# Optimization experiments

Hardware: AMD Instinct MI355X
Metric: run time of the kernel (lower is better)

The kernel has to match this reference:

```python
import jax, jax.numpy as jnp
import numpy as np

# Standard SMPL kinematic tree parents (kintree_table)
PARENTS = np.array([-1, 0, 0, 0, 1, 2, 3, 4, 5, 6, 7, 8, 9, 9, 9,
                    12, 13, 14, 16, 17, 18, 19, 20, 21])
NV, NJ, NB, NP = 6890, 24, 10, 207


def rodrigues(r):
    """Axis-angle [N,3] -> rotation matrices [N,3,3] (Rodrigues formula)."""
    theta = jnp.linalg.norm(r, axis=1, keepdims=True) + 1e-8  # [N,1]
    rh = r / theta                                            # [N,3]
    cos = jnp.cos(theta)[..., None]                           # [N,1,1]
    sin = jnp.sin(theta)[..., None]
    z = jnp.zeros_like(rh[:, 0])
    m = jnp.stack([z, -rh[:, 2], rh[:, 1],
                   rh[:, 2], z, -rh[:, 0],
                   -rh[:, 1], rh[:, 0], z], axis=1).reshape(-1, 3, 3)
    dot = rh[:, :, None] * rh[:, None, :]                     # outer product
    eye = jnp.eye(3, dtype=r.dtype)
    return cos * eye + (1.0 - cos) * dot + sin * m


def setup_inputs() -> dict:
    key = jax.random.key(0)
    ks = jax.random.split(key, 9)
    B = 512
    betas = jax.random.normal(ks[0], (B, NB), dtype=jnp.float32)
    thetas = jax.random.normal(ks[1], (B, NJ * 3), dtype=jnp.float32) * 0.3
    trans = jax.random.normal(ks[2], (B, 3), dtype=jnp.float32)
    scale = jnp.ones((1,), dtype=jnp.float32)
    v_template = jax.random.normal(ks[3], (NV, 3), dtype=jnp.float32)
    shapedirs = jax.random.normal(ks[4], (NV, 3, NB), dtype=jnp.float32) * 0.01
    posedirs = jax.random.normal(ks[5], (NV, 3, NP), dtype=jnp.float32) * 0.01
    Jr = jax.random.uniform(ks[6], (NJ, NV), dtype=jnp.float32)
    J_regressor = Jr / jnp.sum(Jr, axis=1, keepdims=True)
    w = jax.random.uniform(ks[7], (NV, NJ), dtype=jnp.float32)
    weights = w / jnp.sum(w, axis=1, keepdims=True)
    return {"betas": betas, "thetas": thetas, "trans": trans, "scale": scale,
            "v_template": v_template, "shapedirs": shapedirs,
            "posedirs": posedirs, "J_regressor": J_regressor,
            "weights": weights}


def reference(betas, thetas, trans, scale, v_template, shapedirs, posedirs,
              J_regressor, weights):
    B = betas.shape[0]
    dt = betas.dtype
    # Shape blend shapes: v_shaped [B, 6890, 3]
    v_shaped = jnp.einsum('bs,vcs->bvc', betas, shapedirs) + v_template
    # Rest-pose joints J(beta): [B, 24, 3]
    J = jnp.einsum('jv,bvc->bjc', J_regressor, v_shaped)
    # Local rotations from axis-angle, root scaled by `scale`
    lRs = rodrigues(thetas.reshape(-1, 3)).reshape(B, NJ, 3, 3)
    lRs = lRs.at[:, 0].multiply(scale[0])
    # Local joint offsets: root keeps J[:,0], children use J[i] - J[parent[i]]
    parents = jnp.asarray(PARENTS)
    t = J - J[:, jnp.clip(parents, 0)]
    t = t.at[:, 0].set(J[:, 0])
    # Local 4x4 transforms [B, 24, 4, 4]
    top = jnp.concatenate([lRs, t[..., None]], axis=3)          # [B,24,3,4]
    bottom = jnp.broadcast_to(jnp.array([0., 0., 0., 1.], dtype=dt),
                              (B, NJ, 1, 4))
    A = jnp.concatenate([top, bottom], axis=2)
    # Kinematic chain accumulation (fixed 24-joint tree)
    results = [A[:, 0]]
    for i in range(1, NJ):
        results.append(results[PARENTS[i]] @ A[:, i])
    stacked = jnp.stack(results, axis=1)                         # [B,24,4,4]
    # Remove rest-pose joint locations from translation column
    Jh = jnp.concatenate([J, jnp.zeros((B, NJ, 1), dtype=dt)], axis=2)
    deformed = jnp.einsum('bjxy,bjy->bjx', stacked, Jh)          # [B,24,4]
    G = stacked.at[..., 3].add(-deformed)
    # Pose blend shapes from non-root rotations
    lrotmin = (lRs[:, 1:] - jnp.eye(3, dtype=dt)).reshape(B, -1)  # [B,207]
    v_posed = v_shaped + jnp.einsum('bp,vcp->bvc', lrotmin, posedirs)
    # Linear blend skinning
    T = jnp.einsum('bjxy,vj->bvxy', G, weights)                  # [B,6890,4,4]
    vh = jnp.concatenate([v_posed, jnp.ones((B, NV, 1), dtype=dt)], axis=2)
    v = jnp.einsum('bvxy,bvy->bvx', T, vh)[:, :, :3]
    result = v + trans[:, None, :]
    joints = jnp.einsum('jv,bvc->bjc', J_regressor, result)
    return result, joints
```

## Files before the change

### kernel.cpp

```cpp
#include <hip/hip_runtime.h>

#define NVERT 6890
#define NJNT  24
#define NBETA 10
#define NPOSE 207
#define NBATCH 512
#define KPAD 224
#define MROWS 20736
#define NVC (NVERT * 3)

typedef __attribute__((ext_vector_type(8))) short short8;
typedef __attribute__((ext_vector_type(4))) float floatx4;

__constant__ int c_par[NJNT]   = {-1,0,0,0,1,2,3,4,5,6,7,8,9,9,9,12,13,14,16,17,18,19,20,21};
__constant__ int c_depth[NJNT] = { 0,1,1,1,2,2,2,3,3,3,4,4,4,4,4,5,5,5,6,6,7,7,8,8};

static __device__ __forceinline__ unsigned short f2bf(float x) {
  union { float f; unsigned u; } v; v.f = x;
  unsigned r = (v.u + 0x7FFFu + ((v.u >> 16) & 1u)) >> 16;
  return (unsigned short)r;
}
static __device__ __forceinline__ float bf2f(unsigned short h) {
  union { unsigned u; float f; } v; v.u = (unsigned)h << 16;
  return v.f;
}

__global__ __launch_bounds__(256) void k_buildA(
    const float* __restrict__ pdir, const float* __restrict__ sd,
    const float* __restrict__ vt, unsigned short* __restrict__ AT) {
  const int idx = blockIdx.x * 256 + threadIdx.x;
  const int row = idx / KPAD, k = idx - row * KPAD;
  float val = 0.f;
  if (row < NVC) {
    if (k < NPOSE)            val = pdir[(size_t)row * NPOSE + k];
    else if (k < NPOSE + 10)  val = sd[(size_t)row * 10 + (k - NPOSE)];
    else if (k == NPOSE + 10) val = vt[row];
  }
  AT[idx] = f2bf(val);
}

__global__ __launch_bounds__(256) void k_buildW(
    const float* __restrict__ wgt, unsigned short* __restrict__ W16) {
  const int idx = blockIdx.x * 256 + threadIdx.x;
  const int v = idx >> 6, c = idx & 63, j = c & 31, h = c >> 5;
  const float w = (v < NVERT && j < 24) ? wgt[(size_t)v * 24 + j] : 0.f;
  const unsigned short hi = f2bf(w);
  W16[idx] = h ? f2bf(w - bf2f(hi)) : hi;
}

__global__ __launch_bounds__(256) void k_jreg1(
    const float* __restrict__ Jr, const float* __restrict__ vt,
    const float* __restrict__ sd, float* __restrict__ wsJP) {
  const int jc = blockIdx.x, j = jc / 3, c = jc % 3;
  const int v0 = blockIdx.y * 864;
  const int vend = min(NVERT, v0 + 864);
  const int tid = threadIdx.x;
  float acc[11];
  #pragma unroll
  for (int k = 0; k < 11; ++k) acc[k] = 0.f;
  for (int v = v0 + tid; v < vend; v += 256) {
    const float w = Jr[j * NVERT + v];
    acc[0] += w * vt[v * 3 + c];
    const float* s = sd + (size_t)v * 30 + c * 10;
    #pragma unroll
    for (int k = 0; k < 10; ++k) acc[1 + k] += w * s[k];
  }
  #pragma unroll
  for (int off = 32; off > 0; off >>= 1) {
    #pragma unroll
    for (int k = 0; k < 11; ++k) acc[k] += __shfl_down(acc[k], off, 64);
  }
  __shared__ float red[4][11];
  const int lane = tid & 63, wv = tid >> 6;
  if (lane == 0) {
    #pragma unroll
    for (int k = 0; k < 11; ++k) red[wv][k] = acc[k];
  }
  __syncthreads();
  if (tid == 0) {
    #pragma unroll
    for (int k = 0; k < 11; ++k)
      wsJP[(size_t)(blockIdx.y * 72 + jc) * 11 + k] =
          red[0][k] + red[1][k] + red[2][k] + red[3][k];
  }
}

__global__ __launch_bounds__(256, 2) void k_chain3(
    const float* __restrict__ betas, const float* __restrict__ thetas,
    const float* __restrict__ scale, const float* __restrict__ trans,
    const float* __restrict__ wsJP,
    unsigned short* __restrict__ BT, unsigned short* __restrict__ G16) {
  __shared__ __align__(16) float sJ[792];
  __shared__ __align__(16) float sJJ[4][72];
  __shared__ __align__(16) float sM[4][288];
  __shared__ __align__(16) unsigned short sG[4][1024];
  __shared__ __align__(16) unsigned short sB[4][KPAD];

  const int tid = threadIdx.x;
  const int wv = tid >> 6, lane = tid & 63;
  const int b = blockIdx.x * 4 + wv;

  if (tid < 72) {
    #pragma unroll
    for (int k = 0; k < 11; ++k) {
      float s = 0.f;
      #pragma unroll
      for (int c8 = 0; c8 < 8; ++c8) s += wsJP[(size_t)(c8 * 72 + tid) * 11 + k];
      if (k == 0) sJ[tid] = s;
      else        sJ[72 + tid * 10 + (k - 1)] = s;
    }
  }
  #pragma unroll
  for (int r = 0; r < 4; ++r) {
    sG[wv][lane * 16 + r * 4 + 0] = 0; sG[wv][lane * 16 + r * 4 + 1] = 0;
    sG[wv][lane * 16 + r * 4 + 2] = 0; sG[wv][lane * 16 + r * 4 + 3] = 0;
  }
  __syncthreads();

  float R[9], t[3], M[12], Jx = 0.f, Jy = 0.f, Jz = 0.f;
  const int i = lane;
  if (i < NJNT) {
    #pragma unroll
    for (int c = 0; c < 3; ++c) {
      float a = sJ[i * 3 + c];
      const float* d = sJ + 72 + (i * 3 + c) * 10;
      #pragma unroll
      for (int s = 0; s < NBETA; ++s) a += d[s] * betas[b * NBETA + s];
      if (c == 0) Jx = a; else if (c == 1) Jy = a; else Jz = a;
    }
    sJJ[wv][i * 3 + 0] = Jx; sJJ[wv][i * 3 + 1] = Jy; sJJ[wv][i * 3 + 2] = Jz;
    const float rx = thetas[b * 72 + i * 3 + 0];
    const float ry = thetas[b * 72 + i * 3 + 1];
    const float rz = thetas[b * 72 + i * 3 + 2];
    const float th = sqrtf(rx * rx + ry * ry + rz * rz) + 1e-8f;
    const float inv = 1.f / th;
    const float x = rx * inv, y = ry * inv, z = rz * inv;
    const float cs = cosf(th), sn = sinf(th), omc = 1.f - cs;
    R[0] = cs + omc * x * x;     R[1] = omc * x * y - sn * z; R[2] = omc * x * z + sn * y;
    R[3] = omc * x * y + sn * z; R[4] = cs + omc * y * y;     R[5] = omc * y * z - sn * x;
    R[6] = omc * x * z - sn * y; R[7] = omc * y * z + sn * x; R[8] = cs + omc * z * z;
    if (i == 0) {
      const float sc = scale[0];
      #pragma unroll
      for (int k = 0; k < 9; ++k) R[k] *= sc;
    } else {
      #pragma unroll
      for (int k = 0; k < 9; ++k)
        sB[wv][(i - 1) * 9 + k] = f2bf(R[k] - ((k == 0 || k == 4 || k == 8) ? 1.f : 0.f));
    }
  }
  if (i == 0) {
    #pragma unroll
    for (int s = 0; s < NBETA; ++s) sB[wv][NPOSE + s] = f2bf(betas[b * NBETA + s]);
    sB[wv][NPOSE + 10] = 0x3F80;
    #pragma unroll
    for (int k = NPOSE + 11; k < KPAD; ++k) sB[wv][k] = 0;
  }
  __syncthreads();

  if (i < NJNT) {
    if (i == 0) { t[0] = Jx; t[1] = Jy; t[2] = Jz; }
    else {
      const int p = c_par[i];
      t[0] = Jx - sJJ[wv][p * 3 + 0];
      t[1] = Jy - sJJ[wv][p * 3 + 1];
      t[2] = Jz - sJJ[wv][p * 3 + 2];
    }
    if (i == 0) {
      #pragma unroll
      for (int r = 0; r < 3; ++r) {
        M[r*4+0] = R[r*3+0]; M[r*4+1] = R[r*3+1]; M[r*4+2] = R[r*3+2]; M[r*4+3] = t[r];
      }
      #pragma unroll
      for (int k = 0; k < 12; ++k) sM[wv][k] = M[k];
    }
  }
  __syncthreads();

  for (int lvl = 1; lvl <= 8; ++lvl) {
    if (i < NJNT && c_depth[i] == lvl) {
      const float* Mp = sM[wv] + c_par[i] * 12;
      #pragma unroll
      for (int r = 0; r < 3; ++r) {
        const float p0 = Mp[r*4+0], p1 = Mp[r*4+1], p2 = Mp[r*4+2], p3 = Mp[r*4+3];
        M[r*4+0] = p0*R[0] + p1*R[3] + p2*R[6];
        M[r*4+1] = p0*R[1] + p1*R[4] + p2*R[7];
        M[r*4+2] = p0*R[2] + p1*R[5] + p2*R[8];
        M[r*4+3] = p0*t[0] + p1*t[1] + p2*t[2] + p3;
      }
      #pragma unroll
      for (int k = 0; k < 12; ++k) sM[wv][i * 12 + k] = M[k];
    }
    __syncthreads();
  }

  if (i < NJNT) {
    #pragma unroll
    for (int r = 0; r < 3; ++r) {
      M[r*4+3] = M[r*4+3] - (M[r*4+0]*Jx + M[r*4+1]*Jy + M[r*4+2]*Jz)
               + trans[b * 3 + r];
    }
    #pragma unroll
    for (int e = 0; e < 12; ++e) {
      const float g = M[e];
      const unsigned short hi = f2bf(g);
      sG[wv][e * 32 + i]       = hi;
      sG[wv][512 + e * 32 + i] = f2bf(g - bf2f(hi));
    }
  }
  __syncthreads();

  *(uint4*)(G16 + (size_t)b * 1024 + lane * 16)     = *(uint4*)&sG[wv][lane * 16];
  *(uint4*)(G16 + (size_t)b * 1024 + lane * 16 + 8) = *(uint4*)&sG[wv][lane * 16 + 8];
  if (lane < 28)
    *(uint4*)(BT + (size_t)b * KPAD + lane * 8) = *(uint4*)&sB[wv][lane * 8];
}

__global__ __launch_bounds__(256, 3) void k_skin4(
    const unsigned short* __restrict__ AT, const unsigned short* __restrict__ BT,
    const unsigned short* __restrict__ W16, const unsigned short* __restrict__ G16,
    float* __restrict__ out) {
  __shared__ __align__(16) char smem[43776];
  unsigned short* sAs = (unsigned short*)smem;
  unsigned short* sBs = (unsigned short*)(smem + 15360);
  float* sV           = (float*)smem;
  unsigned short* sG2 = (unsigned short*)(smem + 13056);
  unsigned short* sWh = (unsigned short*)(smem + 33536);
  unsigned short* sWl = (unsigned short*)(smem + 38656);

  const int tid = threadIdx.x;
  const int wv = tid >> 6, lane = tid & 63;
  const int q = lane >> 4, n = lane & 15;
  const int b0 = blockIdx.x * 64;
  const int vc0 = blockIdx.y * 192;

  for (int i = tid; i < 512; i += 256) {
    const int row = i >> 3, c8 = i & 7;
    const uint4 w = *(const uint4*)(W16 + (size_t)(blockIdx.y * 64 + row) * 64 + c8 * 8);
    if (c8 < 4) *(uint4*)(sWh + row * 40 + c8 * 8) = w;
    else        *(uint4*)(sWl + row * 40 + (c8 - 4) * 8) = w;
  }

  floatx4 acc[3][4];
  #pragma unroll
  for (int mt = 0; mt < 3; ++mt)
    #pragma unroll
    for (int nt = 0; nt < 4; ++nt) acc[mt][nt] = (floatx4)(0.f);

  const int srow = tid >> 2, sj = tid & 3;
  for (int kt = 0; kt < 7; ++kt) {
    if (kt) __syncthreads();
    #pragma unroll
    for (int it = 0; it < 3; ++it) {
      const int row = it * 64 + srow;
      *(uint4*)(sAs + row * 40 + sj * 8) =
          *(const uint4*)(AT + (size_t)(vc0 + row) * KPAD + kt * 32 + sj * 8);
    }
    *(uint4*)(sBs + srow * 40 + sj * 8) =
        *(const uint4*)(BT + (size_t)(b0 + srow) * KPAD + kt * 32 + sj * 8);
    __syncthreads();
    short8 af[3], bfr[4];
    #pragma unroll
    for (int mt = 0; mt < 3; ++mt)
      af[mt] = *(const short8*)(sAs + (48 * wv + 16 * mt + n) * 40 + q * 8);
    #pragma unroll
    for (int nt = 0; nt < 4; ++nt)
      bfr[nt] = *(const short8*)(sBs + (16 * nt + n) * 40 + q * 8);
    #pragma unroll
    for (int mt = 0; mt < 3; ++mt)
      #pragma unroll
      for (int nt = 0; nt < 4; ++nt)
        acc[mt][nt] = __builtin_amdgcn_mfma_f32_16x16x32_bf16(
            af[mt], bfr[nt], acc[mt][nt], 0, 0, 0);
  }

  short8 wh[4], wl[4];
  #pragma unroll
  for (int vt = 0; vt < 4; ++vt) {
    wh[vt] = *(const short8*)(sWh + (vt * 16 + n) * 40 + q * 8);
    wl[vt] = *(const short8*)(sWl + (vt * 16 + n) * 40 + q * 8);
  }

  for (int nt = 0; nt < 4; ++nt) {
    for (int s = 0; s < 2; ++s) {
      __syncthreads();
      if (s == 0) {
        #pragma unroll
        for (int mt = 0; mt < 3; ++mt)
          #pragma unroll
          for (int r = 0; r < 4; ++r)
            sV[(48 * wv + 16 * mt + 4 * q + r) * 17 + n] = acc[mt][nt][r];
      }
      const int bg0 = b0 + nt * 16 + s * 8;
      for (int i = tid; i < 1024; i += 256) {
        const int row = i >> 2, c4 = i & 3;
        const int t = row >> 5, rem = row & 31;
        *(uint4*)(sG2 + row * 40 + c4 * 8) =
            *(const uint4*)(G16 + (size_t)(bg0 + t) * 1024 + rem * 32 + c4 * 8);
      }
      __syncthreads();
      #pragma unroll
      for (int bb = 0; bb < 2; ++bb) {
        const int t = wv * 2 + bb;
        const int col = s * 8 + t;
        const int bg = b0 + nt * 16 + col;
        const short8 gh = *(const short8*)(sG2 + (t * 32 + n) * 40 + q * 8);
        const short8 gl = *(const short8*)(sG2 + (t * 32 + 16 + n) * 40 + q * 8);
        #pragma unroll
        for (int vt = 0; vt < 4; ++vt) {
          floatx4 a2 = (floatx4)(0.f);
          a2 = __builtin_amdgcn_mfma_f32_16x16x32_bf16(gh, wl[vt], a2, 0, 0, 0);
          a2 = __builtin_amdgcn_mfma_f32_16x16x32_bf16(gl, wh[vt], a2, 0, 0, 0);
          a2 = __builtin_amdgcn_mfma_f32_16x16x32_bf16(gh, wh[vt], a2, 0, 0, 0);
          const float X = sV[(48 * vt + 3 * n + 0) * 17 + col];
          const float Y = sV[(48 * vt + 3 * n + 1) * 17 + col];
          const float Z = sV[(48 * vt + 3 * n + 2) * 17 + col];
          const float o = a2[0] * X + a2[1] * Y + a2[2] * Z + a2[3];
          const int vc = vc0 + 48 * vt + 3 * n + q;
          if (q < 3 && vc < NVC)
            out[(size_t)bg * NVC + vc] = o;
        }
      }
    }
  }
}

__global__ __launch_bounds__(256) void k_joints(
    const float* __restrict__ Jr, const float* __restrict__ res,
    float* __restrict__ joints) {
  const int b = blockIdx.x;
  const int lane = threadIdx.x & 63, wv = threadIdx.x >> 6;
  float acc[18];
  #pragma unroll
  for (int k = 0; k < 18; ++k) acc[k] = 0.f;
  const float* rb = res + (size_t)b * NVC;
  for (int v = lane; v < NVERT; v += 64) {
    const float r0 = rb[v*3+0], r1 = rb[v*3+1], r2 = rb[v*3+2];
    #pragma unroll
    for (int k = 0; k < 6; ++k) {
      const int j = wv + 4 * k;
      const float w = Jr[j * NVERT + v];
      acc[k*3+0] += w * r0; acc[k*3+1] += w * r1; acc[k*3+2] += w * r2;
    }
  }
  #pragma unroll
  for (int off = 32; off > 0; off >>= 1) {
    #pragma unroll
    for (int k = 0; k < 18; ++k) acc[k] += __shfl_down(acc[k], off, 64);
  }
  if (lane == 0) {
    #pragma unroll
    for (int k = 0; k < 6; ++k) {
      const int j = wv + 4 * k;
      joints[(size_t)b * 72 + j * 3 + 0] = acc[k*3+0];
      joints[(size_t)b * 72 + j * 3 + 1] = acc[k*3+1];
      joints[(size_t)b * 72 + j * 3 + 2] = acc[k*3+2];
    }
  }
}

extern "C" void kernel_launch(void* const* d_in, const int* in_sizes, int n_in,
                              void* d_out, int out_size, void* d_ws, size_t ws_size,
                              hipStream_t stream) {
  const float* betas  = (const float*)d_in[0];
  const float* thetas = (const float*)d_in[1];
  const float* trans  = (const float*)d_in[2];
  const float* scale  = (const float*)d_in[3];
  const float* vtpl   = (const float*)d_in[4];
  const float* sd     = (const float*)d_in[5];
  const float* pdir   = (const float*)d_in[6];
  const float* Jr     = (const float*)d_in[7];
  const float* wgt    = (const float*)d_in[8];
  float* out = (float*)d_out;

  float* ws   = (float*)d_ws;
  float* wsJP = ws;
  unsigned short* AT  = (unsigned short*)(ws + 6336);
  unsigned short* BT  = AT + (size_t)MROWS * KPAD;
  unsigned short* W16 = BT + (size_t)NBATCH * KPAD;
  unsigned short* G16 = W16 + (size_t)6912 * 64;

  k_buildA<<<(MROWS * KPAD) / 256, 256, 0, stream>>>(pdir, sd, vtpl, AT);
  k_buildW<<<(6912 * 64) / 256, 256, 0, stream>>>(wgt, W16);
  k_jreg1<<<dim3(72, 8), 256, 0, stream>>>(Jr, vtpl, sd, wsJP);
  k_chain3<<<NBATCH / 4, 256, 0, stream>>>(betas, thetas, scale, trans, wsJP, BT, G16);
  k_skin4<<<dim3(8, 108), 256, 0, stream>>>(AT, BT, W16, G16, out);
  k_joints<<<NBATCH, 256, 0, stream>>>(Jr, out, out + (size_t)NBATCH * NVC);
}
```

Baseline: 206.9 us.

## Retile A/B operands by k-tile, register-prefetch tiles, remap block order

The A and B operand matrices are stored k-tile-major, so each 32-wide k-slice is a contiguous block. The GEMM loop now prefetches the next k-tile into registers while the MFMAs run, and the G tiles get the same register double-buffering. The skinning weights are read straight from global memory into registers instead of through LDS, which shrinks shared memory and lets the launch bound rise to 4 blocks. A 1D grid with a swizzled block mapping replaces the 2D grid to change which blocks run together and how they share cache. In exchange, register pressure goes up and the occupancy target may cause spills.

```diff
diff --git a/kernel.cpp b/kernel.cpp
--- a/kernel.cpp
+++ b/kernel.cpp
@@ -29,7 +29,10 @@
     const float* __restrict__ pdir, const float* __restrict__ sd,
     const float* __restrict__ vt, unsigned short* __restrict__ AT) {
   const int idx = blockIdx.x * 256 + threadIdx.x;
-  const int row = idx / KPAD, k = idx - row * KPAD;
+  const int kk = idx & 31;
+  const int row = (idx >> 5) % MROWS;
+  const int kt = idx / (MROWS * 32);
+  const int k = kt * 32 + kk;
   float val = 0.f;
   if (row < NVC) {
     if (k < NPOSE)            val = pdir[(size_t)row * NPOSE + k];
@@ -213,33 +216,29 @@
   *(uint4*)(G16 + (size_t)b * 1024 + lane * 16)     = *(uint4*)&sG[wv][lane * 16];
   *(uint4*)(G16 + (size_t)b * 1024 + lane * 16 + 8) = *(uint4*)&sG[wv][lane * 16 + 8];
   if (lane < 28)
-    *(uint4*)(BT + (size_t)b * KPAD + lane * 8) = *(uint4*)&sB[wv][lane * 8];
-}
-
-__global__ __launch_bounds__(256, 3) void k_skin4(
+    *(uint4*)(BT + ((size_t)(lane >> 2) * NBATCH + b) * 32 + (lane & 3) * 8) =
+        *(uint4*)&sB[wv][lane * 8];
+}
+
+__global__ __launch_bounds__(256, 4) void k_skin4(
     const unsigned short* __restrict__ AT, const unsigned short* __restrict__ BT,
     const unsigned short* __restrict__ W16, const unsigned short* __restrict__ G16,
     float* __restrict__ out) {
-  __shared__ __align__(16) char smem[43776];
+  __shared__ __align__(16) char smem[33536];
   unsigned short* sAs = (unsigned short*)smem;
   unsigned short* sBs = (unsigned short*)(smem + 15360);
   float* sV           = (float*)smem;
   unsigned short* sG2 = (unsigned short*)(smem + 13056);
-  unsigned short* sWh = (unsigned short*)(smem + 33536);
-  unsigned short* sWl = (unsigned short*)(smem + 38656);
 
   const int tid = threadIdx.x;
   const int wv = tid >> 6, lane = tid & 63;
   const int q = lane >> 4, n = lane & 15;
-  const int b0 = blockIdx.x * 64;
-  const int vc0 = blockIdx.y * 192;
-
-  for (int i = tid; i < 512; i += 256) {
-    const int row = i >> 3, c8 = i & 7;
-    const uint4 w = *(const uint4*)(W16 + (size_t)(blockIdx.y * 64 + row) * 64 + c8 * 8);
-    if (c8 < 4) *(uint4*)(sWh + row * 40 + c8 * 8) = w;
-    else        *(uint4*)(sWl + row * 40 + (c8 - 4) * 8) = w;
-  }
+
+  const int fb = blockIdx.x;
+  const int vb = (fb & 7) * 108 + (fb >> 3);
+  const int b0 = (vb & 7) * 64;
+  const int by = vb >> 3;
+  const int vc0 = by * 192;
 
   floatx4 acc[3][4];
   #pragma unroll
@@ -248,17 +247,27 @@
     for (int nt = 0; nt < 4; ++nt) acc[mt][nt] = (floatx4)(0.f);
 
   const int srow = tid >> 2, sj = tid & 3;
+
+  uint4 ra[3], rbq;
+  #pragma unroll
+  for (int it = 0; it < 3; ++it)
+    ra[it] = *(const uint4*)(AT + (size_t)(vc0 + it * 64 + srow) * 32 + sj * 8);
+  rbq = *(const uint4*)(BT + (size_t)(b0 + srow) * 32 + sj * 8);
+
   for (int kt = 0; kt < 7; ++kt) {
     if (kt) __syncthreads();
     #pragma unroll
-    for (int it = 0; it < 3; ++it) {
-      const int row = it * 64 + srow;
-      *(uint4*)(sAs + row * 40 + sj * 8) =
-          *(const uint4*)(AT + (size_t)(vc0 + row) * KPAD + kt * 32 + sj * 8);
-    }
-    *(uint4*)(sBs + srow * 40 + sj * 8) =
-        *(const uint4*)(BT + (size_t)(b0 + srow) * KPAD + kt * 32 + sj * 8);
+    for (int it = 0; it < 3; ++it)
+      *(uint4*)(sAs + (it * 64 + srow) * 40 + sj * 8) = ra[it];
+    *(uint4*)(sBs + srow * 40 + sj * 8) = rbq;
     __syncthreads();
+    if (kt < 6) {
+      #pragma unroll
+      for (int it = 0; it < 3; ++it)
+        ra[it] = *(const uint4*)(AT +
+            ((size_t)(kt + 1) * MROWS + vc0 + it * 64 + srow) * 32 + sj * 8);
+      rbq = *(const uint4*)(BT + ((size_t)(kt + 1) * NBATCH + b0 + srow) * 32 + sj * 8);
+    }
     short8 af[3], bfr[4];
     #pragma unroll
     for (int mt = 0; mt < 3; ++mt)
@@ -277,8 +286,18 @@
   short8 wh[4], wl[4];
   #pragma unroll
   for (int vt = 0; vt < 4; ++vt) {
-    wh[vt] = *(const short8*)(sWh + (vt * 16 + n) * 40 + q * 8);
-    wl[vt] = *(const short8*)(sWl + (vt * 16 + n) * 40 + q * 8);
+    const unsigned short* wr = W16 + (size_t)(by * 64 + vt * 16 + n) * 64;
+    wh[vt] = *(const short8*)(wr + q * 8);
+    wl[vt] = *(const short8*)(wr + 32 + q * 8);
+  }
+
+  uint4 gr[4];
+  #pragma unroll
+  for (int c = 0; c < 4; ++c) {
+    const int i = tid + c * 256;
+    const int row = i >> 2, c4 = i & 3;
+    const int t = row >> 5, rem = row & 31;
+    gr[c] = *(const uint4*)(G16 + (size_t)(b0 + t) * 1024 + rem * 32 + c4 * 8);
   }
 
   for (int nt = 0; nt < 4; ++nt) {
@@ -291,14 +310,24 @@
           for (int r = 0; r < 4; ++r)
             sV[(48 * wv + 16 * mt + 4 * q + r) * 17 + n] = acc[mt][nt][r];
       }
-      const int bg0 = b0 + nt * 16 + s * 8;
-      for (int i = tid; i < 1024; i += 256) {
+      #pragma unroll
+      for (int c = 0; c < 4; ++c) {
+        const int i = tid + c * 256;
         const int row = i >> 2, c4 = i & 3;
-        const int t = row >> 5, rem = row & 31;
-        *(uint4*)(sG2 + row * 40 + c4 * 8) =
-            *(const uint4*)(G16 + (size_t)(bg0 + t) * 1024 + rem * 32 + c4 * 8);
+        *(uint4*)(sG2 + row * 40 + c4 * 8) = gr[c];
       }
       __syncthreads();
+      const int rnd = nt * 2 + s;
+      if (rnd < 7) {
+        const int bg0n = b0 + ((rnd + 1) >> 1) * 16 + ((rnd + 1) & 1) * 8;
+        #pragma unroll
+        for (int c = 0; c < 4; ++c) {
+          const int i = tid + c * 256;
+          const int row = i >> 2, c4 = i & 3;
+          const int t = row >> 5, rem = row & 31;
+          gr[c] = *(const uint4*)(G16 + (size_t)(bg0n + t) * 1024 + rem * 32 + c4 * 8);
+        }
+      }
       #pragma unroll
       for (int bb = 0; bb < 2; ++bb) {
         const int t = wv * 2 + bb;
@@ -384,6 +413,6 @@
   k_buildW<<<(6912 * 64) / 256, 256, 0, stream>>>(wgt, W16);
   k_jreg1<<<dim3(72, 8), 256, 0, stream>>>(Jr, vtpl, sd, wsJP);
   k_chain3<<<NBATCH / 4, 256, 0, stream>>>(betas, thetas, scale, trans, wsJP, BT, G16);
-  k_skin4<<<dim3(8, 108), 256, 0, stream>>>(AT, BT, W16, G16, out);
+  k_skin4<<<864, 256, 0, stream>>>(AT, BT, W16, G16, out);
   k_joints<<<NBATCH, 256, 0, stream>>>(Jr, out, out + (size_t)NBATCH * NVC);
 }
```

Measured after the change: 236.8 us. +14.4%, slower.

## Tile AT/BT layouts by K-slab, remap skin blocks, load weights directly

Applied to the files above, without the earlier changes.

The pose/shape operand matrices AT and BT are stored K-slab-major (32-wide slabs contiguous across rows), so each k-iteration of the skinning GEMM reads one contiguous region. The skinning grid becomes 1D, with a block-index remap intended to spread or group vertex tiles across XCDs/L2. Skinning weights are read straight from global memory into registers instead of being staged through LDS, which shrinks shared memory and could raise occupancy. The risks are uncoalesced weight fragment loads and a buildA index calculation that now uses modulo and division.

```diff
diff --git a/kernel.cpp b/kernel.cpp
--- a/kernel.cpp
+++ b/kernel.cpp
@@ -29,7 +29,10 @@
     const float* __restrict__ pdir, const float* __restrict__ sd,
     const float* __restrict__ vt, unsigned short* __restrict__ AT) {
   const int idx = blockIdx.x * 256 + threadIdx.x;
-  const int row = idx / KPAD, k = idx - row * KPAD;
+  const int kk = idx & 31;
+  const int row = (idx >> 5) % MROWS;
+  const int kt = idx / (MROWS * 32);
+  const int k = kt * 32 + kk;
   float val = 0.f;
   if (row < NVC) {
     if (k < NPOSE)            val = pdir[(size_t)row * NPOSE + k];
@@ -213,33 +216,29 @@
   *(uint4*)(G16 + (size_t)b * 1024 + lane * 16)     = *(uint4*)&sG[wv][lane * 16];
   *(uint4*)(G16 + (size_t)b * 1024 + lane * 16 + 8) = *(uint4*)&sG[wv][lane * 16 + 8];
   if (lane < 28)
-    *(uint4*)(BT + (size_t)b * KPAD + lane * 8) = *(uint4*)&sB[wv][lane * 8];
+    *(uint4*)(BT + ((size_t)(lane >> 2) * NBATCH + b) * 32 + (lane & 3) * 8) =
+        *(uint4*)&sB[wv][lane * 8];
 }
 
 __global__ __launch_bounds__(256, 3) void k_skin4(
     const unsigned short* __restrict__ AT, const unsigned short* __restrict__ BT,
     const unsigned short* __restrict__ W16, const unsigned short* __restrict__ G16,
     float* __restrict__ out) {
-  __shared__ __align__(16) char smem[43776];
+  __shared__ __align__(16) char smem[33536];
   unsigned short* sAs = (unsigned short*)smem;
   unsigned short* sBs = (unsigned short*)(smem + 15360);
   float* sV           = (float*)smem;
   unsigned short* sG2 = (unsigned short*)(smem + 13056);
-  unsigned short* sWh = (unsigned short*)(smem + 33536);
-  unsigned short* sWl = (unsigned short*)(smem + 38656);
 
   const int tid = threadIdx.x;
   const int wv = tid >> 6, lane = tid & 63;
   const int q = lane >> 4, n = lane & 15;
-  const int b0 = blockIdx.x * 64;
-  const int vc0 = blockIdx.y * 192;
-
-  for (int i = tid; i < 512; i += 256) {
-    const int row = i >> 3, c8 = i & 7;
-    const uint4 w = *(const uint4*)(W16 + (size_t)(blockIdx.y * 64 + row) * 64 + c8 * 8);
-    if (c8 < 4) *(uint4*)(sWh + row * 40 + c8 * 8) = w;
-    else        *(uint4*)(sWl + row * 40 + (c8 - 4) * 8) = w;
-  }
+
+  const int fb = blockIdx.x;
+  const int vb = (fb & 7) * 108 + (fb >> 3);
+  const int b0 = (vb & 7) * 64;
+  const int by = vb >> 3;
+  const int vc0 = by * 192;
 
   floatx4 acc[3][4];
   #pragma unroll
@@ -248,16 +247,15 @@
     for (int nt = 0; nt < 4; ++nt) acc[mt][nt] = (floatx4)(0.f);
 
   const int srow = tid >> 2, sj = tid & 3;
+
   for (int kt = 0; kt < 7; ++kt) {
     if (kt) __syncthreads();
     #pragma unroll
-    for (int it = 0; it < 3; ++it) {
-      const int row = it * 64 + srow;
-      *(uint4*)(sAs + row * 40 + sj * 8) =
-          *(const uint4*)(AT + (size_t)(vc0 + row) * KPAD + kt * 32 + sj * 8);
-    }
+    for (int it = 0; it < 3; ++it)
+      *(uint4*)(sAs + (it * 64 + srow) * 40 + sj * 8) =
+          *(const uint4*)(AT + ((size_t)kt * MROWS + vc0 + it * 64 + srow) * 32 + sj * 8);
     *(uint4*)(sBs + srow * 40 + sj * 8) =
-        *(const uint4*)(BT + (size_t)(b0 + srow) * KPAD + kt * 32 + sj * 8);
+        *(const uint4*)(BT + ((size_t)kt * NBATCH + b0 + srow) * 32 + sj * 8);
     __syncthreads();
     short8 af[3], bfr[4];
     #pragma unroll
@@ -277,8 +275,9 @@
   short8 wh[4], wl[4];
   #pragma unroll
   for (int vt = 0; vt < 4; ++vt) {
-    wh[vt] = *(const short8*)(sWh + (vt * 16 + n) * 40 + q * 8);
-    wl[vt] = *(const short8*)(sWl + (vt * 16 + n) * 40 + q * 8);
+    const unsigned short* wr = W16 + (size_t)(by * 64 + vt * 16 + n) * 64;
+    wh[vt] = *(const short8*)(wr + q * 8);
+    wl[vt] = *(const short8*)(wr + 32 + q * 8);
   }
 
   for (int nt = 0; nt < 4; ++nt) {
@@ -384,6 +383,6 @@
   k_buildW<<<(6912 * 64) / 256, 256, 0, stream>>>(wgt, W16);
   k_jreg1<<<dim3(72, 8), 256, 0, stream>>>(Jr, vtpl, sd, wsJP);
   k_chain3<<<NBATCH / 4, 256, 0, stream>>>(betas, thetas, scale, trans, wsJP, BT, G16);
-  k_skin4<<<dim3(8, 108), 256, 0, stream>>>(AT, BT, W16, G16, out);
+  k_skin4<<<864, 256, 0, stream>>>(AT, BT, W16, G16, out);
   k_joints<<<NBATCH, 256, 0, stream>>>(Jr, out, out + (size_t)NBATCH * NVC);
 }
```

Result: faster. 186.6 us (-9.8%).
